# Kernel tuning notes

Measured on AMD Instinct MI355X. Metric: run time of the kernel, lower is better.

## Reference

```python
import jax, jax.numpy as jnp
import numpy as np

EPS = 1e-5

def _bn(x, g, b, m, v):
    return (x - m) * jax.lax.rsqrt(v + EPS) * g + b

def setup_inputs() -> dict:
    key = jax.random.key(0)
    ks = jax.random.split(key, 40)
    B, D, H, O = 4096, 1723 * 6, 1024, 24 * 9 + 10
    d = {"x": jax.random.normal(ks[0], (B, D), jnp.float32)}
    def lin(i, din, dout):
        return (jax.random.normal(ks[i], (din, dout), jnp.float32) * (1.0 / np.sqrt(din)),
                jax.random.normal(ks[i + 1], (dout,), jnp.float32) * 0.01)
    def bnp(i, dout):
        return (jax.random.normal(ks[i], (dout,), jnp.float32) * 0.1 + 1.0,
                jax.random.normal(ks[i + 1], (dout,), jnp.float32) * 0.1,
                jax.random.normal(ks[i + 2], (dout,), jnp.float32) * 0.1,
                jax.random.uniform(ks[i + 3], (dout,), jnp.float32, 0.5, 1.5))
    d["W1"], d["b1"] = lin(1, D, H); d["g1"], d["be1"], d["m1"], d["v1"] = bnp(3, H)
    d["Wa"], d["ba"] = lin(7, H, H); d["ga"], d["bea"], d["ma"], d["va"] = bnp(9, H)
    d["Wb"], d["bb"] = lin(13, H, H); d["gb"], d["beb"], d["mb"], d["vb"] = bnp(15, H)
    d["Wc"], d["bc"] = lin(19, H, H); d["gc"], d["bec"], d["mc"], d["vc"] = bnp(21, H)
    d["Wd"], d["bd"] = lin(25, H, H); d["gd"], d["bed"], d["md"], d["vd"] = bnp(27, H)
    d["Wf"], d["bf"] = lin(31, H, O)
    return d

def reference(x, W1, b1, g1, be1, m1, v1,
              Wa, ba, ga, bea, ma, va,
              Wb, bb, gb, beb, mb, vb,
              Wc, bc, gc, bec, mc, vc,
              Wd, bd, gd, bed, md, vd,
              Wf, bf):
    B = x.shape[0]
    # FCBlock: Linear -> BN -> ReLU
    h = jax.nn.relu(_bn(x @ W1 + b1, g1, be1, m1, v1))
    # FCResBlock 1: relu(h + BN(Linear(relu(BN(Linear(h))))))
    t = jax.nn.relu(_bn(h @ Wa + ba, ga, bea, ma, va))
    t = _bn(t @ Wb + bb, gb, beb, mb, vb)
    h = jax.nn.relu(h + t)
    # FCResBlock 2
    t = jax.nn.relu(_bn(h @ Wc + bc, gc, bec, mc, vc))
    t = _bn(t @ Wd + bd, gd, bed, md, vd)
    h = jax.nn.relu(h + t)
    out = h @ Wf + bf  # [B, 226]
    rot = out[:, :216].reshape(-1, 3, 3)  # [B*24, 3, 3]
    betas = out[:, 216:]                   # [B, 10]
    U, S, Vh = jnp.linalg.svd(rot)         # batched 3x3 SVD
    R = jnp.matmul(U, Vh)                  # U V^T, closest orthogonal matrix
    det = jax.lax.stop_gradient(jnp.linalg.det(R))[:, None, None]  # torch computes det under no_grad
    R = (R * det).reshape(B, 24, 3, 3)
    return (R, betas)
```

## Files before the change

### kernel.cpp

```cpp
#include <hip/hip_runtime.h>
#include <hip/hip_bf16.h>

typedef unsigned int u32;
typedef unsigned short u16;
typedef _Float16 f16;
typedef __attribute__((ext_vector_type(8))) f16 f16x8;
typedef __attribute__((ext_vector_type(4))) float f32x4;
typedef __attribute__((ext_vector_type(4))) u16 u16x4;

#define NB 4096
#define DIN 10338
#define DPAD 10368
#define KC 5184
#define HD 1024
#define OD 226
#define OPAD 256
#define BN_EPS 1e-5f
#define RSC 0.00048828125f

__device__ __forceinline__ u16 f2h(float v) {
  f16 h = (f16)v;
  u16 r;
  __builtin_memcpy(&r, &h, 2);
  return r;
}
__device__ __forceinline__ void split2(float a, u16& s0, u16& s1) {
  f16 h0 = (f16)a;
  float r = (a - (float)h0) * 2048.0f;
  __builtin_memcpy(&s0, &h0, 2);
  s1 = f2h(r);
}

__device__ __forceinline__ void gload_lds16(const u16* g, u16* l) {
  __builtin_amdgcn_global_load_lds(
      (const __attribute__((address_space(1))) u32*)g,
      (__attribute__((address_space(3))) u32*)l, 16, 0, 0);
}

__global__ __launch_bounds__(256) void k_split_x(const float* __restrict__ x,
                                                 f16* __restrict__ p0,
                                                 f16* __restrict__ p1) {
  u32 idx = (blockIdx.x * 256u + threadIdx.x) * 4u;
  u32 row = idx / DPAD;
  u32 col = idx - row * DPAD;
  const float* s = x + (size_t)row * DIN + col;
  float v[4];
#pragma unroll
  for (int i = 0; i < 4; i++) {
    v[i] = ((int)col + i < DIN) ? s[i] : 0.f;
  }
  u16x4 o0, o1;
#pragma unroll
  for (int i = 0; i < 4; i++) {
    u16 a0, a1;
    split2(v[i], a0, a1);
    o0[i] = a0;
    o1[i] = a1;
  }
  *(u16x4*)((u16*)p0 + idx) = o0;
  *(u16x4*)((u16*)p1 + idx) = o1;
}

__global__ __launch_bounds__(256) void k_split_w(const float* __restrict__ W,
                                                 f16* __restrict__ p0,
                                                 f16* __restrict__ p1, int K,
                                                 int N, int Kp) {
  __shared__ float tile[32][33];
  int k0 = blockIdx.x * 32, n0 = blockIdx.y * 32;
  int tx = threadIdx.x, ty = threadIdx.y;
#pragma unroll
  for (int i = 0; i < 4; i++) {
    int k = k0 + ty + i * 8, n = n0 + tx;
    tile[ty + i * 8][tx] = (k < K && n < N) ? W[(size_t)k * N + n] : 0.f;
  }
  __syncthreads();
#pragma unroll
  for (int i = 0; i < 4; i++) {
    int n = n0 + ty + i * 8, k = k0 + tx;
    u16 s0, s1;
    split2(tile[tx][ty + i * 8], s0, s1);
    size_t o = (size_t)n * Kp + k;
    ((u16*)p0)[o] = s0;
    ((u16*)p1)[o] = s1;
  }
}

__global__ __launch_bounds__(512, 2) void k_gemm_big(
    const f16* __restrict__ A0p, const f16* __restrict__ A1p,
    const f16* __restrict__ B0p, const f16* __restrict__ B1p,
    float* __restrict__ P, int ldA, int ldB, int nk) {
  __shared__ __align__(16) u16 lds[3 * 24576];

  const u32 gx = gridDim.x, gy = gridDim.y;
  const u32 nwg = gx * gy * gridDim.z;
  u32 lin = blockIdx.x + gx * (blockIdx.y + gy * blockIdx.z);
  {
    const u32 q = nwg >> 3, r = nwg & 7;
    const u32 xcd = lin & 7, o = lin >> 3;
    lin = (xcd < r ? xcd * (q + 1) : r * (q + 1) + (xcd - r) * q) + o;
  }
  const u32 bz = lin / (gx * gy);
  const u32 rem = lin - bz * gx * gy;
  const u32 by = rem / gx;
  const u32 bx = rem - by * gx;
  const int m0 = by * 256, n0 = bx * 128;
  const size_t kbase = (size_t)bz * KC;

  const u16* __restrict__ A0u = (const u16*)A0p + kbase;
  const u16* __restrict__ A1u = (const u16*)A1p + kbase;
  const u16* __restrict__ B0u = (const u16*)B0p + kbase;
  const u16* __restrict__ B1u = (const u16*)B1p + kbase;
  float* __restrict__ Pz = P + (size_t)bz * NB * HD;

  const int t = threadIdx.x;
  const int lane = t & 63;
  const int wid = t >> 6;
  const int wm = wid >> 1, wn = wid & 1;
  const int l15 = lane & 15, l4 = lane >> 4;

  const int sgc = (((t & 3) ^ ((t >> 3) & 3)) << 3);
  const size_t gA0 = (size_t)(m0 + (t >> 2)) * ldA + sgc;
  const size_t gA1 = gA0 + (size_t)128 * ldA;
  const size_t gB = (size_t)(n0 + (t >> 2)) * ldB + sgc;
  const int dA0 = t * 8, dA1 = 4096 + t * 8, dB = t * 8;

  int offA[4], offB[4];
#pragma unroll
  for (int mi = 0; mi < 4; mi++) {
    int row = wm * 64 + mi * 16 + l15;
    offA[mi] = row * 32 + ((l4 ^ ((row >> 1) & 3)) << 3);
  }
#pragma unroll
  for (int ni = 0; ni < 4; ni++) {
    int row = wn * 64 + ni * 16 + l15;
    offB[ni] = row * 32 + ((l4 ^ ((row >> 1) & 3)) << 3);
  }

  f32x4 hi[4][4], lo[4][4];
#pragma unroll
  for (int i = 0; i < 4; i++)
#pragma unroll
    for (int j = 0; j < 4; j++) {
      f32x4 z = {0.f, 0.f, 0.f, 0.f};
      hi[i][j] = z;
      lo[i][j] = z;
    }

#define STAGEB(buf, kt)                                      \
  {                                                          \
    u16* Sb = lds + (buf) * 24576;                           \
    const size_t ko = (size_t)(kt) * 32;                     \
    gload_lds16(A0u + gA0 + ko, Sb + dA0);                   \
    gload_lds16(A0u + gA1 + ko, Sb + 512 * 8 + dA0);         \
    gload_lds16(A1u + gA0 + ko, Sb + 8192 + dA0);            \
    gload_lds16(A1u + gA1 + ko, Sb + 8192 + 512 * 8 + dA0);  \
    gload_lds16(B0u + gB + ko, Sb + 16384 + dB);             \
    gload_lds16(B1u + gB + ko, Sb + 20480 + dB);             \
  }

#define COMPUTE(Lb)                                                       \
  {                                                                       \
    f16x8 a0[4], a1[4], b0[4], b1[4];                                     \
    _Pragma("unroll") for (int mi = 0; mi < 4; mi++) {                    \
      a0[mi] = *(const f16x8*)((Lb) + offA[mi]);                          \
      a1[mi] = *(const f16x8*)((Lb) + 8192 + offA[mi]);                   \
    }                                                                     \
    _Pragma("unroll") for (int ni = 0; ni < 4; ni++) {                    \
      b0[ni] = *(const f16x8*)((Lb) + 16384 + offB[ni]);                  \
      b1[ni] = *(const f16x8*)((Lb) + 20480 + offB[ni]);                  \
    }                                                                     \
    __builtin_amdgcn_s_setprio(1);                                        \
    _Pragma("unroll") for (int mi = 0; mi < 4; mi++)                      \
        _Pragma("unroll") for (int ni = 0; ni < 4; ni++)                  \
            hi[mi][ni] = __builtin_amdgcn_mfma_f32_16x16x32_f16(          \
                a0[mi], b0[ni], hi[mi][ni], 0, 0, 0);                     \
    _Pragma("unroll") for (int mi = 0; mi < 4; mi++)                      \
        _Pragma("unroll") for (int ni = 0; ni < 4; ni++)                  \
            lo[mi][ni] = __builtin_amdgcn_mfma_f32_16x16x32_f16(          \
                a0[mi], b1[ni], lo[mi][ni], 0, 0, 0);                     \
    _Pragma("unroll") for (int mi = 0; mi < 4; mi++)                      \
        _Pragma("unroll") for (int ni = 0; ni < 4; ni++)                  \
            lo[mi][ni] = __builtin_amdgcn_mfma_f32_16x16x32_f16(          \
                a1[mi], b0[ni], lo[mi][ni], 0, 0, 0);                     \
    __builtin_amdgcn_s_setprio(0);                                        \
  }

  STAGEB(0, 0)
  STAGEB(1, 1)
  asm volatile("s_waitcnt vmcnt(6)" ::: "memory");
  __builtin_amdgcn_s_barrier();
  __builtin_amdgcn_sched_barrier(0);

  for (int tau = 0; tau < nk - 2; ++tau) {
    const u16* Lb = lds + (tau % 3) * 24576;
    STAGEB((tau + 2) % 3, tau + 2)
    COMPUTE(Lb)
    asm volatile("s_waitcnt vmcnt(6)" ::: "memory");
    __builtin_amdgcn_s_barrier();
    __builtin_amdgcn_sched_barrier(0);
  }
  asm volatile("s_waitcnt vmcnt(0)" ::: "memory");
  __builtin_amdgcn_s_barrier();
  __builtin_amdgcn_sched_barrier(0);
#pragma unroll 1
  for (int tau = nk - 2; tau < nk; ++tau) {
    const u16* Lb = lds + (tau % 3) * 24576;
    COMPUTE(Lb)
  }
#undef STAGEB
#undef COMPUTE

  const int rowb = m0 + wm * 64 + l4 * 4;
  const int colb = n0 + wn * 64 + l15;
#pragma unroll
  for (int mi = 0; mi < 4; mi++) {
#pragma unroll
    for (int ni = 0; ni < 4; ni++) {
      const int col = colb + ni * 16;
#pragma unroll
      for (int r = 0; r < 4; r++) {
        const int row = rowb + mi * 16 + r;
        Pz[(size_t)row * HD + col] = hi[mi][ni][r] + lo[mi][ni][r] * RSC;
      }
    }
  }
}

__global__ __launch_bounds__(256) void k_epi1(
    const float* __restrict__ P0, const float* __restrict__ P1,
    const float* __restrict__ bias, const float* __restrict__ gam,
    const float* __restrict__ bet, const float* __restrict__ mu,
    const float* __restrict__ var, float* __restrict__ hF,
    f16* __restrict__ h0, f16* __restrict__ h1) {
  const u32 i4 = (blockIdx.x * 256u + threadIdx.x) * 4u;
  const u32 col0 = i4 & (HD - 1);
  f32x4 a = *(const f32x4*)(P0 + i4);
  f32x4 b = *(const f32x4*)(P1 + i4);
  f32x4 y;
  u16x4 o0, o1;
#pragma unroll
  for (int e = 0; e < 4; e++) {
    const u32 c = col0 + e;
    float sc = gam[c] * rsqrtf(var[c] + BN_EPS);
    float v = ((a[e] + b[e]) + bias[c] - mu[c]) * sc + bet[c];
    v = fmaxf(v, 0.f);
    y[e] = v;
    u16 s0, s1;
    split2(v, s0, s1);
    o0[e] = s0;
    o1[e] = s1;
  }
  *(f32x4*)(hF + i4) = y;
  *(u16x4*)((u16*)h0 + i4) = o0;
  *(u16x4*)((u16*)h1 + i4) = o1;
}

template <int EPI>
__global__ __launch_bounds__(512, 2) void k_gemm_f(
    const f16* __restrict__ A0p, const f16* __restrict__ A1p,
    const f16* __restrict__ B0p, const f16* __restrict__ B1p,
    const float* __restrict__ bias, const float* __restrict__ gam,
    const float* __restrict__ bet, const float* __restrict__ mu,
    const float* __restrict__ var, const float* __restrict__ resF,
    float* __restrict__ hFout, f16* __restrict__ pl0, f16* __restrict__ pl1,
    float* __restrict__ oF, int ldA, int ldB, int nk, int ldout) {
  __shared__ __align__(16) u16 lds[4 * 16384];

  const u32 gx = gridDim.x, gy = gridDim.y;
  const u32 nwg = gx * gy;
  u32 lin = blockIdx.x + gx * blockIdx.y;
  {
    const u32 q = nwg >> 3, r = nwg & 7;
    const u32 xcd = lin & 7, o = lin >> 3;
    lin = (xcd < r ? xcd * (q + 1) : r * (q + 1) + (xcd - r) * q) + o;
  }
  const u32 by = lin / gx;
  const u32 bx = lin - by * gx;
  const int m0 = by * 128, n0 = bx * 128;

  const u16* __restrict__ A0u = (const u16*)A0p;
  const u16* __restrict__ A1u = (const u16*)A1p;
  const u16* __restrict__ B0u = (const u16*)B0p;
  const u16* __restrict__ B1u = (const u16*)B1p;

  const int t = threadIdx.x;
  const int lane = t & 63;
  const int wid = t >> 6;
  const int wm = wid >> 1, wn = wid & 1;
  const int l15 = lane & 15, l4 = lane >> 4;

  const int srow = t >> 2, sj = t & 3;
  const int sgc = ((sj ^ ((srow >> 1) & 3)) << 3);
  const size_t gA = (size_t)(m0 + srow) * ldA + sgc;
  const size_t gB = (size_t)(n0 + srow) * ldB + sgc;
  const int d0 = t * 8;

  int offA[2], offB[4];
#pragma unroll
  for (int mi = 0; mi < 2; mi++) {
    int row = wm * 32 + mi * 16 + l15;
    offA[mi] = row * 32 + ((l4 ^ ((row >> 1) & 3)) << 3);
  }
#pragma unroll
  for (int ni = 0; ni < 4; ni++) {
    int row = wn * 64 + ni * 16 + l15;
    offB[ni] = row * 32 + ((l4 ^ ((row >> 1) & 3)) << 3);
  }

  f32x4 hi[2][4], lo[2][4];
#pragma unroll
  for (int i = 0; i < 2; i++)
#pragma unroll
    for (int j = 0; j < 4; j++) {
      f32x4 z = {0.f, 0.f, 0.f, 0.f};
      hi[i][j] = z;
      lo[i][j] = z;
    }

#define STAGE(buf, kt)                                        \
  {                                                           \
    u16* Sb = lds + (buf) * 16384;                            \
    const size_t ko = (size_t)(kt) * 32;                      \
    gload_lds16(A0u + gA + ko, Sb + d0);                      \
    gload_lds16(A1u + gA + ko, Sb + 4096 + d0);               \
    gload_lds16(B0u + gB + ko, Sb + 8192 + d0);               \
    gload_lds16(B1u + gB + ko, Sb + 12288 + d0);              \
  }

#define COMPUTE2(Lb)                                                      \
  {                                                                       \
    f16x8 a0[2], a1[2], b0[4], b1[4];                                     \
    _Pragma("unroll") for (int mi = 0; mi < 2; mi++) {                    \
      a0[mi] = *(const f16x8*)((Lb) + offA[mi]);                          \
      a1[mi] = *(const f16x8*)((Lb) + 4096 + offA[mi]);                   \
    }                                                                     \
    _Pragma("unroll") for (int ni = 0; ni < 4; ni++) {                    \
      b0[ni] = *(const f16x8*)((Lb) + 8192 + offB[ni]);                   \
      b1[ni] = *(const f16x8*)((Lb) + 12288 + offB[ni]);                  \
    }                                                                     \
    __builtin_amdgcn_s_setprio(1);                                        \
    _Pragma("unroll") for (int mi = 0; mi < 2; mi++)                      \
        _Pragma("unroll") for (int ni = 0; ni < 4; ni++)                  \
            hi[mi][ni] = __builtin_amdgcn_mfma_f32_16x16x32_f16(          \
                a0[mi], b0[ni], hi[mi][ni], 0, 0, 0);                     \
    _Pragma("unroll") for (int mi = 0; mi < 2; mi++)                      \
        _Pragma("unroll") for (int ni = 0; ni < 4; ni++)                  \
            lo[mi][ni] = __builtin_amdgcn_mfma_f32_16x16x32_f16(          \
                a0[mi], b1[ni], lo[mi][ni], 0, 0, 0);                     \
    _Pragma("unroll") for (int mi = 0; mi < 2; mi++)                      \
        _Pragma("unroll") for (int ni = 0; ni < 4; ni++)                  \
            lo[mi][ni] = __builtin_amdgcn_mfma_f32_16x16x32_f16(          \
                a1[mi], b0[ni], lo[mi][ni], 0, 0, 0);                     \
    __builtin_amdgcn_s_setprio(0);                                        \
  }

  STAGE(0, 0)
  STAGE(1, 1)
  STAGE(2, 2)
  asm volatile("s_waitcnt vmcnt(8)" ::: "memory");
  __builtin_amdgcn_s_barrier();
  __builtin_amdgcn_sched_barrier(0);

  for (int tau = 0; tau < nk - 3; ++tau) {
    const u16* Lb = lds + (tau & 3) * 16384;
    STAGE((tau + 3) & 3, tau + 3)
    COMPUTE2(Lb)
    asm volatile("s_waitcnt vmcnt(8)" ::: "memory");
    __builtin_amdgcn_s_barrier();
    __builtin_amdgcn_sched_barrier(0);
  }
  asm volatile("s_waitcnt vmcnt(0)" ::: "memory");
  __builtin_amdgcn_s_barrier();
  __builtin_amdgcn_sched_barrier(0);
#pragma unroll 1
  for (int tau = nk - 3; tau < nk; ++tau) {
    const u16* Lb = lds + (tau & 3) * 16384;
    COMPUTE2(Lb)
  }
#undef STAGE
#undef COMPUTE2

  const int rowb = m0 + wm * 32 + l4 * 4;
  const int colb = n0 + wn * 64 + l15;
#pragma unroll
  for (int ni = 0; ni < 4; ni++) {
    const int col = colb + ni * 16;
    float sc = 1.f, pb = 0.f;
    if (EPI == 4) {
      pb = (col < OD) ? bias[col] : 0.f;
    } else {
      sc = gam[col] * rsqrtf(var[col] + BN_EPS);
      pb = (bias[col] - mu[col]) * sc + bet[col];
    }
#pragma unroll
    for (int mi = 0; mi < 2; mi++) {
#pragma unroll
      for (int r = 0; r < 4; r++) {
        const int row = rowb + mi * 16 + r;
        float s = hi[mi][ni][r] + lo[mi][ni][r] * RSC;
        if (EPI == 4) {
          oF[(size_t)row * ldout + col] = s + pb;
          continue;
        }
        float v = s * sc + pb;
        if (EPI == 2 || EPI == 3) v += resF[(size_t)row * HD + col];
        v = fmaxf(v, 0.f);
        if (EPI == 2) hFout[(size_t)row * HD + col] = v;
        u16 s0, s1;
        split2(v, s0, s1);
        size_t o = (size_t)row * HD + col;
        ((u16*)pl0)[o] = s0;
        ((u16*)pl1)[o] = s1;
      }
    }
  }
}

__global__ __launch_bounds__(256) void k_polar(const float* __restrict__ oF,
                                               float* __restrict__ R) {
  int g = blockIdx.x * 256 + threadIdx.x;
  if (g >= NB * 24) return;
  int b = g / 24, j = g - b * 24;
  const float* p = oF + (size_t)b * OPAD + j * 9;
  float xv[9];
#pragma unroll
  for (int e = 0; e < 9; e++) xv[e] = p[e];
#pragma unroll 1
  for (int it = 0; it < 18; it++) {
    float c0 = xv[4] * xv[8] - xv[5] * xv[7];
    float c1 = xv[5] * xv[6] - xv[3] * xv[8];
    float c2 = xv[3] * xv[7] - xv[4] * xv[6];
    float c3 = xv[2] * xv[7] - xv[1] * xv[8];
    float c4 = xv[0] * xv[8] - xv[2] * xv[6];
    float c5 = xv[1] * xv[6] - xv[0] * xv[7];
    float c6 = xv[1] * xv[5] - xv[2] * xv[4];
    float c7 = xv[2] * xv[3] - xv[0] * xv[5];
    float c8 = xv[0] * xv[4] - xv[1] * xv[3];
    float det = xv[0] * c0 + xv[1] * c1 + xv[2] * c2;
    if (fabsf(det) < 1e-30f) break;
    float inv = 1.f / det;
    float y0 = c0 * inv, y1 = c1 * inv, y2 = c2 * inv;
    float y3 = c3 * inv, y4 = c4 * inv, y5 = c5 * inv;
    float y6 = c6 * inv, y7 = c7 * inv, y8 = c8 * inv;
    float gmm = 1.f;
    if (it < 8) {
      float nx = xv[0]*xv[0]+xv[1]*xv[1]+xv[2]*xv[2]+xv[3]*xv[3]+xv[4]*xv[4]
               + xv[5]*xv[5]+xv[6]*xv[6]+xv[7]*xv[7]+xv[8]*xv[8];
      float ny = y0*y0+y1*y1+y2*y2+y3*y3+y4*y4+y5*y5+y6*y6+y7*y7+y8*y8;
      gmm = sqrtf(sqrtf(ny / nx));
    }
    float a0 = 0.5f * gmm, a1 = 0.5f / gmm;
    xv[0] = a0 * xv[0] + a1 * y0; xv[1] = a0 * xv[1] + a1 * y1;
    xv[2] = a0 * xv[2] + a1 * y2; xv[3] = a0 * xv[3] + a1 * y3;
    xv[4] = a0 * xv[4] + a1 * y4; xv[5] = a0 * xv[5] + a1 * y5;
    xv[6] = a0 * xv[6] + a1 * y6; xv[7] = a0 * xv[7] + a1 * y7;
    xv[8] = a0 * xv[8] + a1 * y8;
  }
  float dfin = xv[0] * (xv[4] * xv[8] - xv[5] * xv[7])
             + xv[1] * (xv[5] * xv[6] - xv[3] * xv[8])
             + xv[2] * (xv[3] * xv[7] - xv[4] * xv[6]);
  float s = (dfin > 0.f) ? 1.f : -1.f;
  float* q = R + (size_t)g * 9;
#pragma unroll
  for (int e = 0; e < 9; e++) q[e] = s * xv[e];
}

__global__ __launch_bounds__(256) void k_betas(const float* __restrict__ oF,
                                               float* __restrict__ dst) {
  int i = blockIdx.x * 256 + threadIdx.x;
  if (i >= NB * 10) return;
  int b = i / 10, j = i - b * 10;
  dst[i] = oF[(size_t)b * OPAD + 216 + j];
}

extern "C" void kernel_launch(void* const* d_in, const int* in_sizes, int n_in,
                              void* d_out, int out_size, void* d_ws, size_t ws_size,
                              hipStream_t stream) {
  const float* x   = (const float*)d_in[0];
  const float* W1  = (const float*)d_in[1];
  const float* b1  = (const float*)d_in[2];
  const float* g1  = (const float*)d_in[3];
  const float* be1 = (const float*)d_in[4];
  const float* m1  = (const float*)d_in[5];
  const float* v1  = (const float*)d_in[6];
  const float* Wa  = (const float*)d_in[7];
  const float* ba  = (const float*)d_in[8];
  const float* ga  = (const float*)d_in[9];
  const float* bea = (const float*)d_in[10];
  const float* ma  = (const float*)d_in[11];
  const float* va  = (const float*)d_in[12];
  const float* Wb  = (const float*)d_in[13];
  const float* bb  = (const float*)d_in[14];
  const float* gb  = (const float*)d_in[15];
  const float* beb = (const float*)d_in[16];
  const float* mb  = (const float*)d_in[17];
  const float* vb  = (const float*)d_in[18];
  const float* Wc  = (const float*)d_in[19];
  const float* bc  = (const float*)d_in[20];
  const float* gc  = (const float*)d_in[21];
  const float* bec = (const float*)d_in[22];
  const float* mc  = (const float*)d_in[23];
  const float* vc  = (const float*)d_in[24];
  const float* Wd  = (const float*)d_in[25];
  const float* bd  = (const float*)d_in[26];
  const float* gd  = (const float*)d_in[27];
  const float* bed = (const float*)d_in[28];
  const float* md  = (const float*)d_in[29];
  const float* vd  = (const float*)d_in[30];
  const float* Wf  = (const float*)d_in[31];
  const float* bf  = (const float*)d_in[32];
  (void)in_sizes; (void)n_in; (void)out_size; (void)ws_size;

  char* ws = (char*)d_ws;
  size_t off = 0;
  auto alloc = [&](size_t bytes) -> void* {
    void* p = ws + off;
    off += (bytes + 255) & ~(size_t)255;
    return p;
  };
  f16* xp0 = (f16*)alloc((size_t)NB * DPAD * 2);
  f16* xp1 = (f16*)alloc((size_t)NB * DPAD * 2);
  f16* w1p0 = (f16*)alloc((size_t)HD * DPAD * 2);
  f16* w1p1 = (f16*)alloc((size_t)HD * DPAD * 2);
  f16* wap0 = (f16*)alloc((size_t)HD * HD * 2);
  f16* wap1 = (f16*)alloc((size_t)HD * HD * 2);
  f16* wbp0 = (f16*)alloc((size_t)HD * HD * 2);
  f16* wbp1 = (f16*)alloc((size_t)HD * HD * 2);
  f16* wcp0 = (f16*)alloc((size_t)HD * HD * 2);
  f16* wcp1 = (f16*)alloc((size_t)HD * HD * 2);
  f16* wdp0 = (f16*)alloc((size_t)HD * HD * 2);
  f16* wdp1 = (f16*)alloc((size_t)HD * HD * 2);
  f16* wfp0 = (f16*)alloc((size_t)OPAD * HD * 2);
  f16* wfp1 = (f16*)alloc((size_t)OPAD * HD * 2);
  float* P = (float*)alloc((size_t)2 * NB * HD * 4);
  f16* h0 = (f16*)xp0;
  f16* h1 = h0 + (size_t)NB * HD;
  f16* t0 = h1 + (size_t)NB * HD;
  f16* t1 = t0 + (size_t)NB * HD;
  float* hF = (float*)(t1 + (size_t)NB * HD);
  float* oF = hF + (size_t)NB * HD;

  k_split_x<<<NB * DPAD / 4 / 256, 256, 0, stream>>>(x, xp0, xp1);
  dim3 tb(32, 8);
  k_split_w<<<dim3(DPAD / 32, HD / 32), tb, 0, stream>>>(W1, w1p0, w1p1, DIN, HD, DPAD);
  k_split_w<<<dim3(HD / 32, HD / 32), tb, 0, stream>>>(Wa, wap0, wap1, HD, HD, HD);
  k_split_w<<<dim3(HD / 32, HD / 32), tb, 0, stream>>>(Wb, wbp0, wbp1, HD, HD, HD);
  k_split_w<<<dim3(HD / 32, HD / 32), tb, 0, stream>>>(Wc, wcp0, wcp1, HD, HD, HD);
  k_split_w<<<dim3(HD / 32, HD / 32), tb, 0, stream>>>(Wd, wdp0, wdp1, HD, HD, HD);
  k_split_w<<<dim3(HD / 32, OPAD / 32), tb, 0, stream>>>(Wf, wfp0, wfp1, HD, OD, HD);

  dim3 g1g(HD / 128, NB / 256, 2);
  dim3 gg(HD / 128, NB / 128);
  dim3 gf(OPAD / 128, NB / 128);

  k_gemm_big<<<g1g, 512, 0, stream>>>(xp0, xp1, w1p0, w1p1, P, DPAD, DPAD,
                                      KC / 32);
  k_epi1<<<NB * HD / 4 / 256, 256, 0, stream>>>(P, P + (size_t)NB * HD, b1, g1,
                                                be1, m1, v1, hF, h0, h1);
  k_gemm_f<1><<<gg, 512, 0, stream>>>(
      h0, h1, wap0, wap1, ba, ga, bea, ma, va, nullptr, nullptr, t0, t1,
      nullptr, HD, HD, HD / 32, HD);
  k_gemm_f<2><<<gg, 512, 0, stream>>>(
      t0, t1, wbp0, wbp1, bb, gb, beb, mb, vb, hF, hF, h0, h1, nullptr, HD,
      HD, HD / 32, HD);
  k_gemm_f<1><<<gg, 512, 0, stream>>>(
      h0, h1, wcp0, wcp1, bc, gc, bec, mc, vc, nullptr, nullptr, t0, t1,
      nullptr, HD, HD, HD / 32, HD);
  k_gemm_f<3><<<gg, 512, 0, stream>>>(
      t0, t1, wdp0, wdp1, bd, gd, bed, md, vd, hF, nullptr, h0, h1, nullptr,
      HD, HD, HD / 32, HD);
  k_gemm_f<4><<<gf, 512, 0, stream>>>(
      h0, h1, wfp0, wfp1, bf, nullptr, nullptr, nullptr, nullptr, nullptr,
      nullptr, nullptr, nullptr, oF, HD, HD, HD / 32, OPAD);

  float* Rout = (float*)d_out;
  k_polar<<<(NB * 24 + 255) / 256, 256, 0, stream>>>(oF, Rout);
  k_betas<<<(NB * 10 + 255) / 256, 256, 0, stream>>>(oF, Rout + (size_t)NB * 216);
}
```

Before: 526.2 us.

## Split GEMM k-step into three phases interleaving LDS reads, global prefetch and MFMA

Both the big split-K GEMM kernel and the smaller hidden-layer GEMM kernel now divide each k-iteration into three phases. Each phase loads a subset of fragments from LDS, issues part of the next stage's global-to-LDS loads, synchronises, then runs one block of MFMAs. This spreads memory issue across the compute and reuses a register buffer (xf) to lower register pressure. In exchange it adds extra workgroup barriers per iteration, which could stall waves.

```diff
diff --git a/kernel.cpp b/kernel.cpp
--- a/kernel.cpp
+++ b/kernel.cpp
@@ -122,7 +122,7 @@
   const size_t gA0 = (size_t)(m0 + (t >> 2)) * ldA + sgc;
   const size_t gA1 = gA0 + (size_t)128 * ldA;
   const size_t gB = (size_t)(n0 + (t >> 2)) * ldB + sgc;
-  const int dA0 = t * 8, dA1 = 4096 + t * 8, dB = t * 8;
+  const int dA0 = t * 8, dB = t * 8;
 
   int offA[4], offB[4];
 #pragma unroll
@@ -146,58 +146,76 @@
       lo[i][j] = z;
     }
 
-#define STAGEB(buf, kt)                                      \
-  {                                                          \
-    u16* Sb = lds + (buf) * 24576;                           \
-    const size_t ko = (size_t)(kt) * 32;                     \
-    gload_lds16(A0u + gA0 + ko, Sb + dA0);                   \
-    gload_lds16(A0u + gA1 + ko, Sb + 512 * 8 + dA0);         \
-    gload_lds16(A1u + gA0 + ko, Sb + 8192 + dA0);            \
-    gload_lds16(A1u + gA1 + ko, Sb + 8192 + 512 * 8 + dA0);  \
-    gload_lds16(B0u + gB + ko, Sb + 16384 + dB);             \
-    gload_lds16(B1u + gB + ko, Sb + 20480 + dB);             \
-  }
-
-#define COMPUTE(Lb)                                                       \
-  {                                                                       \
-    f16x8 a0[4], a1[4], b0[4], b1[4];                                     \
-    _Pragma("unroll") for (int mi = 0; mi < 4; mi++) {                    \
-      a0[mi] = *(const f16x8*)((Lb) + offA[mi]);                          \
-      a1[mi] = *(const f16x8*)((Lb) + 8192 + offA[mi]);                   \
-    }                                                                     \
-    _Pragma("unroll") for (int ni = 0; ni < 4; ni++) {                    \
-      b0[ni] = *(const f16x8*)((Lb) + 16384 + offB[ni]);                  \
-      b1[ni] = *(const f16x8*)((Lb) + 20480 + offB[ni]);                  \
-    }                                                                     \
-    __builtin_amdgcn_s_setprio(1);                                        \
-    _Pragma("unroll") for (int mi = 0; mi < 4; mi++)                      \
-        _Pragma("unroll") for (int ni = 0; ni < 4; ni++)                  \
-            hi[mi][ni] = __builtin_amdgcn_mfma_f32_16x16x32_f16(          \
-                a0[mi], b0[ni], hi[mi][ni], 0, 0, 0);                     \
-    _Pragma("unroll") for (int mi = 0; mi < 4; mi++)                      \
-        _Pragma("unroll") for (int ni = 0; ni < 4; ni++)                  \
-            lo[mi][ni] = __builtin_amdgcn_mfma_f32_16x16x32_f16(          \
-                a0[mi], b1[ni], lo[mi][ni], 0, 0, 0);                     \
-    _Pragma("unroll") for (int mi = 0; mi < 4; mi++)                      \
-        _Pragma("unroll") for (int ni = 0; ni < 4; ni++)                  \
-            lo[mi][ni] = __builtin_amdgcn_mfma_f32_16x16x32_f16(          \
-                a1[mi], b0[ni], lo[mi][ni], 0, 0, 0);                     \
-    __builtin_amdgcn_s_setprio(0);                                        \
-  }
-
-  STAGEB(0, 0)
-  STAGEB(1, 1)
+#define STAGE_A0(Sb, ko)                         \
+  gload_lds16(A0u + gA0 + (ko), (Sb) + dA0);     \
+  gload_lds16(A0u + gA1 + (ko), (Sb) + 4096 + dA0);
+#define STAGE_A1(Sb, ko)                              \
+  gload_lds16(A1u + gA0 + (ko), (Sb) + 8192 + dA0);   \
+  gload_lds16(A1u + gA1 + (ko), (Sb) + 12288 + dA0);
+#define STAGE_B(Sb, ko)                               \
+  gload_lds16(B0u + gB + (ko), (Sb) + 16384 + dB);    \
+  gload_lds16(B1u + gB + (ko), (Sb) + 20480 + dB);
+
+#define MFMA16(dst, af, bf)                                              \
+  _Pragma("unroll") for (int mi = 0; mi < 4; mi++)                       \
+      _Pragma("unroll") for (int ni = 0; ni < 4; ni++)                   \
+          dst[mi][ni] = __builtin_amdgcn_mfma_f32_16x16x32_f16(          \
+              af[mi], bf[ni], dst[mi][ni], 0, 0, 0);
+
+  {
+    u16* Sb0 = lds;
+    u16* Sb1 = lds + 24576;
+    STAGE_A0(Sb0, 0) STAGE_A1(Sb0, 0) STAGE_B(Sb0, 0)
+    STAGE_A0(Sb1, 32) STAGE_A1(Sb1, 32) STAGE_B(Sb1, 32)
+  }
   asm volatile("s_waitcnt vmcnt(6)" ::: "memory");
   __builtin_amdgcn_s_barrier();
   __builtin_amdgcn_sched_barrier(0);
 
   for (int tau = 0; tau < nk - 2; ++tau) {
     const u16* Lb = lds + (tau % 3) * 24576;
-    STAGEB((tau + 2) % 3, tau + 2)
-    COMPUTE(Lb)
+    u16* Sb = lds + ((tau + 2) % 3) * 24576;
+    const size_t ko = (size_t)(tau + 2) * 32;
+    f16x8 a0[4], b0[4], xf[4];
+
+#pragma unroll
+    for (int mi = 0; mi < 4; mi++) a0[mi] = *(const f16x8*)(Lb + offA[mi]);
+#pragma unroll
+    for (int ni = 0; ni < 4; ni++)
+      b0[ni] = *(const f16x8*)(Lb + 16384 + offB[ni]);
+    STAGE_A0(Sb, ko)
+    __builtin_amdgcn_s_barrier();
+    asm volatile("s_waitcnt lgkmcnt(0)" ::: "memory");
+    __builtin_amdgcn_sched_barrier(0);
+    __builtin_amdgcn_s_setprio(1);
+    MFMA16(hi, a0, b0)
+    __builtin_amdgcn_s_setprio(0);
+    __builtin_amdgcn_s_barrier();
+
+#pragma unroll
+    for (int ni = 0; ni < 4; ni++)
+      xf[ni] = *(const f16x8*)(Lb + 20480 + offB[ni]);
+    STAGE_A1(Sb, ko)
+    __builtin_amdgcn_s_barrier();
+    asm volatile("s_waitcnt lgkmcnt(0)" ::: "memory");
+    __builtin_amdgcn_sched_barrier(0);
+    __builtin_amdgcn_s_setprio(1);
+    MFMA16(lo, a0, xf)
+    __builtin_amdgcn_s_setprio(0);
+    __builtin_amdgcn_s_barrier();
+
+#pragma unroll
+    for (int mi = 0; mi < 4; mi++)
+      xf[mi] = *(const f16x8*)(Lb + 8192 + offA[mi]);
+    STAGE_B(Sb, ko)
     asm volatile("s_waitcnt vmcnt(6)" ::: "memory");
     __builtin_amdgcn_s_barrier();
+    asm volatile("s_waitcnt lgkmcnt(0)" ::: "memory");
     __builtin_amdgcn_sched_barrier(0);
+    __builtin_amdgcn_s_setprio(1);
+    MFMA16(lo, xf, b0)
+    __builtin_amdgcn_s_setprio(0);
+    __builtin_amdgcn_s_barrier();
   }
   asm volatile("s_waitcnt vmcnt(0)" ::: "memory");
   __builtin_amdgcn_s_barrier();
@@ -205,10 +223,26 @@
 #pragma unroll 1
   for (int tau = nk - 2; tau < nk; ++tau) {
     const u16* Lb = lds + (tau % 3) * 24576;
-    COMPUTE(Lb)
-  }
-#undef STAGEB
-#undef COMPUTE
+    f16x8 a0[4], b0[4], xf[4];
+#pragma unroll
+    for (int mi = 0; mi < 4; mi++) a0[mi] = *(const f16x8*)(Lb + offA[mi]);
+#pragma unroll
+    for (int ni = 0; ni < 4; ni++)
+      b0[ni] = *(const f16x8*)(Lb + 16384 + offB[ni]);
+    MFMA16(hi, a0, b0)
+#pragma unroll
+    for (int ni = 0; ni < 4; ni++)
+      xf[ni] = *(const f16x8*)(Lb + 20480 + offB[ni]);
+    MFMA16(lo, a0, xf)
+#pragma unroll
+    for (int mi = 0; mi < 4; mi++)
+      xf[mi] = *(const f16x8*)(Lb + 8192 + offA[mi]);
+    MFMA16(lo, xf, b0)
+  }
+#undef STAGE_A0
+#undef STAGE_A1
+#undef STAGE_B
+#undef MFMA16
 
   const int rowb = m0 + wm * 64 + l4 * 4;
   const int colb = n0 + wn * 64 + l15;
@@ -317,57 +351,73 @@
       lo[i][j] = z;
     }
 
-#define STAGE(buf, kt)                                        \
-  {                                                           \
-    u16* Sb = lds + (buf) * 16384;                            \
-    const size_t ko = (size_t)(kt) * 32;                      \
-    gload_lds16(A0u + gA + ko, Sb + d0);                      \
-    gload_lds16(A1u + gA + ko, Sb + 4096 + d0);               \
-    gload_lds16(B0u + gB + ko, Sb + 8192 + d0);               \
-    gload_lds16(B1u + gB + ko, Sb + 12288 + d0);              \
-  }
-
-#define COMPUTE2(Lb)                                                      \
-  {                                                                       \
-    f16x8 a0[2], a1[2], b0[4], b1[4];                                     \
-    _Pragma("unroll") for (int mi = 0; mi < 2; mi++) {                    \
-      a0[mi] = *(const f16x8*)((Lb) + offA[mi]);                          \
-      a1[mi] = *(const f16x8*)((Lb) + 4096 + offA[mi]);                   \
-    }                                                                     \
-    _Pragma("unroll") for (int ni = 0; ni < 4; ni++) {                    \
-      b0[ni] = *(const f16x8*)((Lb) + 8192 + offB[ni]);                   \
-      b1[ni] = *(const f16x8*)((Lb) + 12288 + offB[ni]);                  \
-    }                                                                     \
-    __builtin_amdgcn_s_setprio(1);                                        \
-    _Pragma("unroll") for (int mi = 0; mi < 2; mi++)                      \
-        _Pragma("unroll") for (int ni = 0; ni < 4; ni++)                  \
-            hi[mi][ni] = __builtin_amdgcn_mfma_f32_16x16x32_f16(          \
-                a0[mi], b0[ni], hi[mi][ni], 0, 0, 0);                     \
-    _Pragma("unroll") for (int mi = 0; mi < 2; mi++)                      \
-        _Pragma("unroll") for (int ni = 0; ni < 4; ni++)                  \
-            lo[mi][ni] = __builtin_amdgcn_mfma_f32_16x16x32_f16(          \
-                a0[mi], b1[ni], lo[mi][ni], 0, 0, 0);                     \
-    _Pragma("unroll") for (int mi = 0; mi < 2; mi++)                      \
-        _Pragma("unroll") for (int ni = 0; ni < 4; ni++)                  \
-            lo[mi][ni] = __builtin_amdgcn_mfma_f32_16x16x32_f16(          \
-                a1[mi], b0[ni], lo[mi][ni], 0, 0, 0);                     \
-    __builtin_amdgcn_s_setprio(0);                                        \
-  }
-
-  STAGE(0, 0)
-  STAGE(1, 1)
-  STAGE(2, 2)
+#define STG_A0(Sb, ko) gload_lds16(A0u + gA + (ko), (Sb) + d0);
+#define STG_A1(Sb, ko) gload_lds16(A1u + gA + (ko), (Sb) + 4096 + d0);
+#define STG_B(Sb, ko)                               \
+  gload_lds16(B0u + gB + (ko), (Sb) + 8192 + d0);   \
+  gload_lds16(B1u + gB + (ko), (Sb) + 12288 + d0);
+#define MFMA8(dst, af, bf)                                               \
+  _Pragma("unroll") for (int mi = 0; mi < 2; mi++)                       \
+      _Pragma("unroll") for (int ni = 0; ni < 4; ni++)                   \
+          dst[mi][ni] = __builtin_amdgcn_mfma_f32_16x16x32_f16(          \
+              af[mi], bf[ni], dst[mi][ni], 0, 0, 0);
+
+  {
+    u16* S0 = lds;
+    u16* S1 = lds + 16384;
+    u16* S2 = lds + 32768;
+    STG_A0(S0, 0) STG_A1(S0, 0) STG_B(S0, 0)
+    STG_A0(S1, 32) STG_A1(S1, 32) STG_B(S1, 32)
+    STG_A0(S2, 64) STG_A1(S2, 64) STG_B(S2, 64)
+  }
   asm volatile("s_waitcnt vmcnt(8)" ::: "memory");
   __builtin_amdgcn_s_barrier();
   __builtin_amdgcn_sched_barrier(0);
 
   for (int tau = 0; tau < nk - 3; ++tau) {
     const u16* Lb = lds + (tau & 3) * 16384;
-    STAGE((tau + 3) & 3, tau + 3)
-    COMPUTE2(Lb)
+    u16* Sb = lds + ((tau + 3) & 3) * 16384;
+    const size_t ko = (size_t)(tau + 3) * 32;
+    f16x8 a0[2], b0[4], xf[4];
+
+#pragma unroll
+    for (int mi = 0; mi < 2; mi++) a0[mi] = *(const f16x8*)(Lb + offA[mi]);
+#pragma unroll
+    for (int ni = 0; ni < 4; ni++)
+      b0[ni] = *(const f16x8*)(Lb + 8192 + offB[ni]);
+    STG_A0(Sb, ko)
+    __builtin_amdgcn_s_barrier();
+    asm volatile("s_waitcnt lgkmcnt(0)" ::: "memory");
+    __builtin_amdgcn_sched_barrier(0);
+    __builtin_amdgcn_s_setprio(1);
+    MFMA8(hi, a0, b0)
+    __builtin_amdgcn_s_setprio(0);
+    __builtin_amdgcn_s_barrier();
+
+#pragma unroll
+    for (int ni = 0; ni < 4; ni++)
+      xf[ni] = *(const f16x8*)(Lb + 12288 + offB[ni]);
+    STG_A1(Sb, ko)
+    __builtin_amdgcn_s_barrier();
+    asm volatile("s_waitcnt lgkmcnt(0)" ::: "memory");
+    __builtin_amdgcn_sched_barrier(0);
+    __builtin_amdgcn_s_setprio(1);
+    MFMA8(lo, a0, xf)
+    __builtin_amdgcn_s_setprio(0);
+    __builtin_amdgcn_s_barrier();
+
+#pragma unroll
+    for (int mi = 0; mi < 2; mi++)
+      xf[mi] = *(const f16x8*)(Lb + 4096 + offA[mi]);
+    STG_B(Sb, ko)
     asm volatile("s_waitcnt vmcnt(8)" ::: "memory");
     __builtin_amdgcn_s_barrier();
+    asm volatile("s_waitcnt lgkmcnt(0)" ::: "memory");
     __builtin_amdgcn_sched_barrier(0);
+    __builtin_amdgcn_s_setprio(1);
+    MFMA8(lo, xf, b0)
+    __builtin_amdgcn_s_setprio(0);
+    __builtin_amdgcn_s_barrier();
   }
   asm volatile("s_waitcnt vmcnt(0)" ::: "memory");
   __builtin_amdgcn_s_barrier();
@@ -375,10 +425,26 @@
 #pragma unroll 1
   for (int tau = nk - 3; tau < nk; ++tau) {
     const u16* Lb = lds + (tau & 3) * 16384;
-    COMPUTE2(Lb)
-  }
-#undef STAGE
-#undef COMPUTE2
+    f16x8 a0[2], b0[4], xf[4];
+#pragma unroll
+    for (int mi = 0; mi < 2; mi++) a0[mi] = *(const f16x8*)(Lb + offA[mi]);
+#pragma unroll
+    for (int ni = 0; ni < 4; ni++)
+      b0[ni] = *(const f16x8*)(Lb + 8192 + offB[ni]);
+    MFMA8(hi, a0, b0)
+#pragma unroll
+    for (int ni = 0; ni < 4; ni++)
+      xf[ni] = *(const f16x8*)(Lb + 12288 + offB[ni]);
+    MFMA8(lo, a0, xf)
+#pragma unroll
+    for (int mi = 0; mi < 2; mi++)
+      xf[mi] = *(const f16x8*)(Lb + 4096 + offA[mi]);
+    MFMA8(lo, xf, b0)
+  }
+#undef STG_A0
+#undef STG_A1
+#undef STG_B
+#undef MFMA8
 
   const int rowb = m0 + wm * 32 + l4 * 4;
   const int colb = n0 + wn * 64 + l15;
```

New measurement: 523.6 us. No clear change (-0.5%).
